# Kernel optimization log

Hardware: AMD Instinct MI355X
Metric: run time of the kernel (lower is better)

Reference implementation:

```python
import jax, jax.numpy as jnp
import numpy as np

N_Q = 16384; N_S = 16384; NN = 32; F_IN = 128; F_OUT = 256
K = 15; DIM = 3
RADIUS = 10.0
KP_EXTENT_CFG = 1.0      # config.NETWORK.KP_EXTENT (also scales learned offsets)
DENSITY = 5.0            # config.NETWORK.DENSITY_PARAMETER
EXTENT = KP_EXTENT_CFG * RADIUS / DENSITY   # 2.0
K_RADIUS = 1.5 * EXTENT
OFFSET_DIM = DIM * (K - 1)  # modulated=False, version=0 -> 42


def setup_inputs() -> dict:
    key = jax.random.key(0)
    ks = jax.random.split(key, 8)
    query_points = jax.random.uniform(ks[0], (N_Q, DIM), dtype=jnp.float32)
    support_points = jax.random.uniform(ks[1], (N_S, DIM), dtype=jnp.float32)
    neighbors = jax.random.randint(ks[2], (N_Q, NN), 0, N_S)
    features = jax.random.normal(ks[3], (N_S, F_IN), dtype=jnp.float32)
    # kernel points: fixed disposition inside ball of radius 1.5*extent, first point at center
    kp = jax.random.normal(ks[4], (K, DIM), dtype=jnp.float32)
    kp = kp / jnp.linalg.norm(kp, axis=1, keepdims=True) * (0.7 * K_RADIUS)
    K_points = kp.at[0].set(0.0)
    weight = jax.random.normal(ks[5], (K, F_IN, F_OUT), dtype=jnp.float32) / np.sqrt(F_IN)
    deformable_weight = jax.random.normal(ks[6], (K, F_IN, OFFSET_DIM), dtype=jnp.float32) / np.sqrt(F_IN)
    bias = jnp.zeros((OFFSET_DIM,), dtype=jnp.float32)
    return {"query_points": query_points, "support_points": support_points,
            "neighbors": neighbors, "features": features, "K_points": K_points,
            "weight": weight, "deformable_weight": deformable_weight, "bias": bias}


def _gather_neighb(query_points, support_points, neighbors, features):
    # pad with shadow point (far away) and zero feature row, as in KPConv_ops
    sp = jnp.concatenate([support_points, jnp.full((1, DIM), 1e6, support_points.dtype)], 0)
    ft = jnp.concatenate([features, jnp.zeros((1, features.shape[1]), features.dtype)], 0)
    rel = sp[neighbors] - query_points[:, None, :]   # [n, nn, 3]
    nfeat = ft[neighbors]                            # [n, nn, f]
    return rel, nfeat


def _linear_influence(sq_dist):
    # KP_INFLUENCE='linear': relu(1 - d/extent); CONVOLUTION_MODE='sum'
    return jnp.maximum(1.0 - jnp.sqrt(sq_dist) / EXTENT, 0.0)


def reference(query_points, support_points, neighbors, features, K_points,
              weight, deformable_weight, bias):
    rel, nfeat = _gather_neighb(query_points, support_points, neighbors, features)

    # --- rigid KPConv producing offsets (version=0) ---
    d0 = rel[:, :, None, :] - K_points[None, None, :, :]   # [n, nn, K, 3]
    sq0 = jnp.sum(d0 * d0, axis=-1)                        # [n, nn, K]
    w0 = _linear_influence(sq0)
    wf0 = jnp.einsum('enk,enf->ekf', w0, nfeat)            # [n, K, f]
    feat0 = jnp.einsum('ekf,kfo->eo', wf0, deformable_weight) + bias  # [n, 42]

    # not modulated: reshape to offsets, prepend zero offset for center kernel point
    offsets = feat0.reshape(-1, K - 1, DIM)
    offsets = jnp.concatenate([jnp.zeros_like(offsets[:, :1, :]), offsets], axis=1)
    offsets = offsets * KP_EXTENT_CFG                      # [n, K, 3]

    # --- deformable KPConv ---
    def_kp = K_points[None, :, :] + offsets                # [n, K, 3]
    d1 = rel[:, :, None, :] - def_kp[:, None, :, :]        # [n, nn, K, 3]
    sq1 = jnp.sum(d1 * d1, axis=-1)                        # [n, nn, K]
    w1 = _linear_influence(sq1)                            # out-of-range neighbors get 0 weight
    wf1 = jnp.einsum('enk,enf->ekf', w1, nfeat)            # [n, K, f]
    out = jnp.einsum('ekf,kfo->eo', wf1, weight)           # [n, f_out]
    return out
```

## Files before the change

kernel.cpp:

```cpp
#include <hip/hip_runtime.h>
#include <hip/hip_bf16.h>
#include <math.h>

typedef __attribute__((ext_vector_type(8))) short bf16x8;
typedef __attribute__((ext_vector_type(4))) float f32x4;

#define NQ 16384
#define NN 32
#define FI 128
#define FO 256
#define KPN 15
#define OD 42
#define INV_EXT 0.5f

#define WS_FP1    0u
#define WS_FP2    (8u * 1024u * 1024u)
#define WS_BSW    (12u * 1024u * 1024u)
#define WS_DWBH   (13u * 1024u * 1024u)
#define WS_DWBL   (WS_DWBH + 196608u)

static __device__ __forceinline__ unsigned short f2bf(float x) {
    union { __hip_bfloat16 h; unsigned short u; } cv;
    cv.h = __float2bfloat16(x);
    return cv.u;
}
static __device__ __forceinline__ float bf2f(unsigned short h) {
    union { unsigned int u; float f; } cv;
    cv.u = ((unsigned int)h) << 16;
    return cv.f;
}

union U8 { unsigned short u[8]; bf16x8 v; };

__global__ void pre_all(const float* __restrict__ feat,
                        unsigned int* __restrict__ fp1, unsigned int* __restrict__ fp2,
                        const float* __restrict__ w, unsigned short* __restrict__ Bsw,
                        const float* __restrict__ dw,
                        unsigned short* __restrict__ dhi, unsigned short* __restrict__ dlo)
{
    const int b = blockIdx.x, t = threadIdx.x;
    if (b < 1024) {
        const int g  = b * 256 + t;
        const int lq = g & 3;
        const int fp = (g >> 2) & 3;
        const int s  = g >> 4;
        const float4* f4 = (const float4*)feat;
        const float4 A = f4[s * 32 + fp * 8 + lq];
        const float4 C = f4[s * 32 + fp * 8 + 4 + lq];
        const float av[4] = {A.x, A.y, A.z, A.w};
        const float cv[4] = {C.x, C.y, C.z, C.w};
        uint4 p1a, p1c, p2;
        unsigned int* pa = (unsigned int*)&p1a;
        unsigned int* pc = (unsigned int*)&p1c;
        unsigned int* p2p = (unsigned int*)&p2;
        #pragma unroll
        for (int e = 0; e < 4; e++) {
            const unsigned short ha = f2bf(av[e]), hc = f2bf(cv[e]);
            const unsigned short la = f2bf(av[e] - bf2f(ha));
            const unsigned short lc = f2bf(cv[e] - bf2f(hc));
            pa[e]  = (unsigned int)ha | ((unsigned int)la << 16);
            pc[e]  = (unsigned int)hc | ((unsigned int)lc << 16);
            p2p[e] = (unsigned int)ha | ((unsigned int)hc << 16);
        }
        *(uint4*)&fp1[s * 128 + fp * 32 + lq * 4]      = p1a;
        *(uint4*)&fp1[s * 128 + fp * 32 + 16 + lq * 4] = p1c;
        *(uint4*)&fp2[s * 64 + fp * 16 + lq * 4]       = p2;
    } else if (b < 1024 + 256) {
        const int tid = (b - 1024) * 256 + t;
        const int lane = tid & 63;
        const int kt   = (tid >> 6) & 63;
        const int nt   = tid >> 12;
        const int n    = nt * 16 + (lane & 15);
        const int kbase = kt * 32 + (lane >> 4) * 8;
        unsigned int p[4];
        #pragma unroll
        for (int jj = 0; jj < 4; jj++) {
            unsigned int lo, hi;
            {
                const int kk = kbase + 2 * jj;
                const int f = kk >> 4, k = kk & 15;
                lo = (k < KPN) ? f2bf(w[(k * FI + f) * FO + n]) : 0u;
            }
            {
                const int kk = kbase + 2 * jj + 1;
                const int f = kk >> 4, k = kk & 15;
                hi = (k < KPN) ? f2bf(w[(k * FI + f) * FO + n]) : 0u;
            }
            p[jj] = lo | (hi << 16);
        }
        unsigned int* op = (unsigned int*)&Bsw[tid * 8];
        op[0] = p[0]; op[1] = p[1]; op[2] = p[2]; op[3] = p[3];
    } else {
        const int tid = (b - 1280) * 256 + t;
        const int lane = tid & 63;
        const int kt   = (tid >> 6) & 63;
        const int nt   = tid >> 12;
        const int o    = nt * 16 + (lane & 15);
        const int kbase = kt * 32 + (lane >> 4) * 8;
        #pragma unroll
        for (int j = 0; j < 8; j++) {
            const int kf = kbase + j;
            const int f = kf >> 4, k = kf & 15;
            float v = (k < KPN && o < OD) ? dw[(k * FI + f) * OD + o] : 0.f;
            unsigned short h = f2bf(v);
            dhi[tid * 8 + j] = h;
            dlo[tid * 8 + j] = f2bf(v - bf2f(h));
        }
    }
}

__global__ __launch_bounds__(512, 4)
void k_fused(const float* __restrict__ query, const float* __restrict__ support,
             const int* __restrict__ neighbors, const unsigned int* __restrict__ fp1,
             const unsigned int* __restrict__ fp2, const float* __restrict__ kpoints,
             const unsigned short* __restrict__ dwB_hi,
             const unsigned short* __restrict__ dwB_lo,
             const unsigned short* __restrict__ Bsw,
             const float* __restrict__ bias, float* __restrict__ out)
{
    __shared__ unsigned short wf[16384];
    __shared__ float relx[1024], rely[1024], relz[1024];
    __shared__ float dk_s[32 * 45];
    __shared__ unsigned short nbr_s[1024];
    __shared__ float kp_s[48];

    const int t = threadIdx.x;
    const int qbase = blockIdx.x * 32;
    if (t < 45) kp_s[t] = kpoints[t];
    if (t >= 45 && t < 48) kp_s[t] = 0.f;

    #pragma unroll
    for (int ii = 0; ii < 2; ii++) {
        const int i = ii * 512 + t;
        const int e = i >> 5, n = i & 31;
        const int q = qbase + e;
        const int idx = neighbors[q * NN + n];
        nbr_s[i] = (unsigned short)idx;
        relx[i] = support[idx * 3 + 0] - query[q * 3 + 0];
        rely[i] = support[idx * 3 + 1] - query[q * 3 + 1];
        relz[i] = support[idx * 3 + 2] - query[q * 3 + 2];
    }
    __syncthreads();

    const int wave = t >> 6, lane = t & 63;
    const int quad = lane >> 4, low = lane & 15;
    const int kb = (low < KPN) ? low * 3 : 0;

    U8 ah[4], al[4];
    {
        const float kx = kp_s[kb + 0], ky = kp_s[kb + 1], kz = kp_s[kb + 2];
        #pragma unroll
        for (int ei = 0; ei < 4; ei++) {
            const int ee = wave * 4 + ei;
            #pragma unroll
            for (int j = 0; j < 8; j++) {
                const int ni = ee * 32 + quad * 8 + j;
                const float dx = relx[ni] - kx;
                const float dy = rely[ni] - ky;
                const float dz = relz[ni] - kz;
                const float d = sqrtf(dx * dx + dy * dy + dz * dz);
                float w = 1.0f - d * INV_EXT;
                w = (low < KPN && w > 0.f) ? w : 0.f;
                const unsigned short h = f2bf(w);
                ah[ei].u[j] = h;
                al[ei].u[j] = f2bf(w - bf2f(h));
            }
        }
    }

    f32x4 acc = {0.f, 0.f, 0.f, 0.f};
    const int et = (wave >= 3) ? 1 : 0;
    const int nt = wave - et * 3;

    for (int c2 = 0; c2 < 8; c2++) {
        #pragma unroll 2
        for (int ei = 0; ei < 4; ei++) {
            const int ee = wave * 4 + ei;
            union { unsigned int u[4]; bf16x8 v; } bh, bl;
            #pragma unroll
            for (int jj = 0; jj < 4; jj++) {
                const int r0 = nbr_s[ee * 32 + quad * 8 + 2 * jj];
                const int r1 = nbr_s[ee * 32 + quad * 8 + 2 * jj + 1];
                const unsigned int g0 = fp1[r0 * 128 + c2 * 16 + low];
                const unsigned int g1 = fp1[r1 * 128 + c2 * 16 + low];
                bh.u[jj] = __builtin_amdgcn_perm(g1, g0, 0x05040100u);
                bl.u[jj] = __builtin_amdgcn_perm(g1, g0, 0x07060302u);
            }
            f32x4 o = {0.f, 0.f, 0.f, 0.f};
            o = __builtin_amdgcn_mfma_f32_16x16x32_bf16(al[ei].v, bh.v, o, 0, 0, 0);
            o = __builtin_amdgcn_mfma_f32_16x16x32_bf16(ah[ei].v, bl.v, o, 0, 0, 0);
            o = __builtin_amdgcn_mfma_f32_16x16x32_bf16(ah[ei].v, bh.v, o, 0, 0, 0);
            const int cblk = low + (quad >> 1) * 16;
            const int slot = ee ^ low;
            const int hw   = cblk * 256 + slot * 8 + (quad & 1) * 4;
            const unsigned short h0 = f2bf(o[0]), h1 = f2bf(o[1]);
            const unsigned short h2 = f2bf(o[2]), h3 = f2bf(o[3]);
            uint2 ph;
            ph.x = (unsigned int)h0 | ((unsigned int)h1 << 16);
            ph.y = (unsigned int)h2 | ((unsigned int)h3 << 16);
            *(uint2*)&wf[hw] = ph;
            uint2 pl;
            pl.x = (unsigned int)f2bf(o[0] - bf2f(h0)) |
                   ((unsigned int)f2bf(o[1] - bf2f(h1)) << 16);
            pl.y = (unsigned int)f2bf(o[2] - bf2f(h2)) |
                   ((unsigned int)f2bf(o[3] - bf2f(h3)) << 16);
            *(uint2*)&wf[8192 + hw] = pl;
        }
        __syncthreads();
        if (wave < 6) {
            const bf16x8* Bh = (const bf16x8*)dwB_hi;
            const bf16x8* Bl = (const bf16x8*)dwB_lo;
            #pragma unroll 4
            for (int ktl = 0; ktl < 8; ktl++) {
                const int fl   = ktl * 2 + (quad >> 1);
                const int cblk = fl + (quad & 1) * 16;
                const int slot = (et * 16 + low) ^ fl;
                const int hw   = cblk * 256 + slot * 8;
                bf16x8 a_h = *(const bf16x8*)&wf[hw];
                bf16x8 a_l = *(const bf16x8*)&wf[8192 + hw];
                const int ktg = c2 * 8 + ktl;
                bf16x8 b_h = Bh[(nt * 64 + ktg) * 64 + lane];
                bf16x8 b_l = Bl[(nt * 64 + ktg) * 64 + lane];
                acc = __builtin_amdgcn_mfma_f32_16x16x32_bf16(a_l, b_h, acc, 0, 0, 0);
                acc = __builtin_amdgcn_mfma_f32_16x16x32_bf16(a_h, b_l, acc, 0, 0, 0);
                acc = __builtin_amdgcn_mfma_f32_16x16x32_bf16(a_h, b_h, acc, 0, 0, 0);
            }
        } else if (c2 == 0) {
            const int idx2 = (wave - 6) * 64 + lane;
            if (idx2 < 96) dk_s[(idx2 / 3) * 45 + (idx2 % 3)] = kp_s[idx2 % 3];
        }
        __syncthreads();
    }

    if (wave < 6) {
        const int o = nt * 16 + low;
        if (o < OD) {
            const float bo = bias[o] + kp_s[3 + o];
            #pragma unroll
            for (int r = 0; r < 4; r++) {
                const int ee = et * 16 + quad * 4 + r;
                dk_s[ee * 45 + 3 + o] = bo + acc[r];
            }
        }
    }
    __syncthreads();

    U8 af[4];
    #pragma unroll
    for (int ei = 0; ei < 4; ei++) {
        const int ee = wave * 4 + ei;
        const float kx = dk_s[ee * 45 + kb + 0];
        const float ky = dk_s[ee * 45 + kb + 1];
        const float kz = dk_s[ee * 45 + kb + 2];
        #pragma unroll
        for (int j = 0; j < 8; j++) {
            const int ni = ee * 32 + quad * 8 + j;
            const float dx = relx[ni] - kx;
            const float dy = rely[ni] - ky;
            const float dz = relz[ni] - kz;
            const float d = sqrtf(dx * dx + dy * dy + dz * dz);
            float w = 1.0f - d * INV_EXT;
            w = (low < KPN && w > 0.f) ? w : 0.f;
            af[ei].u[j] = f2bf(w);
        }
    }

    f32x4 acc00 = {0,0,0,0}, acc01 = {0,0,0,0};
    f32x4 acc10 = {0,0,0,0}, acc11 = {0,0,0,0};
    const int nt0 = wave * 2, nt1 = nt0 + 1;
    const bf16x8* Bp = (const bf16x8*)Bsw;

    for (int c = 0; c < 4; c++) {
        #pragma unroll
        for (int ei = 0; ei < 4; ei++) {
            const int ee = wave * 4 + ei;
            union { unsigned int u[4]; bf16x8 v; } bA, bB;
            #pragma unroll
            for (int jj = 0; jj < 4; jj++) {
                const int r0 = nbr_s[ee * 32 + quad * 8 + 2 * jj];
                const int r1 = nbr_s[ee * 32 + quad * 8 + 2 * jj + 1];
                const unsigned int d0 = fp2[r0 * 64 + c * 16 + low];
                const unsigned int d1 = fp2[r1 * 64 + c * 16 + low];
                bA.u[jj] = __builtin_amdgcn_perm(d1, d0, 0x05040100u);
                bB.u[jj] = __builtin_amdgcn_perm(d1, d0, 0x07060302u);
            }
            #pragma unroll
            for (int hh2 = 0; hh2 < 2; hh2++) {
                const bf16x8 b = hh2 ? bB.v : bA.v;
                f32x4 o = {0.f, 0.f, 0.f, 0.f};
                o = __builtin_amdgcn_mfma_f32_16x16x32_bf16(af[ei].v, b, o, 0, 0, 0);
                const int fc   = hh2 * 16 + low;
                const int cblk = fc + (quad >> 1) * 32;
                const int slot = ee ^ fc;
                const int hw   = cblk * 256 + slot * 8 + (quad & 1) * 4;
                uint2 ph;
                ph.x = (unsigned int)f2bf(o[0]) | ((unsigned int)f2bf(o[1]) << 16);
                ph.y = (unsigned int)f2bf(o[2]) | ((unsigned int)f2bf(o[3]) << 16);
                *(uint2*)&wf[hw] = ph;
            }
        }
        __syncthreads();
        #pragma unroll 4
        for (int ktl = 0; ktl < 16; ktl++) {
            const int fcq  = ktl * 2 + (quad >> 1);
            const int cblk = fcq + (quad & 1) * 32;
            const int s0 = (low ^ fcq) * 8;
            const int s1 = ((16 + low) ^ fcq) * 8;
            bf16x8 a0 = *(const bf16x8*)&wf[cblk * 256 + s0];
            bf16x8 a1 = *(const bf16x8*)&wf[cblk * 256 + s1];
            const int ktg = c * 16 + ktl;
            bf16x8 b0 = Bp[(nt0 * 64 + ktg) * 64 + lane];
            bf16x8 b1 = Bp[(nt1 * 64 + ktg) * 64 + lane];
            acc00 = __builtin_amdgcn_mfma_f32_16x16x32_bf16(a0, b0, acc00, 0, 0, 0);
            acc01 = __builtin_amdgcn_mfma_f32_16x16x32_bf16(a0, b1, acc01, 0, 0, 0);
            acc10 = __builtin_amdgcn_mfma_f32_16x16x32_bf16(a1, b0, acc10, 0, 0, 0);
            acc11 = __builtin_amdgcn_mfma_f32_16x16x32_bf16(a1, b1, acc11, 0, 0, 0);
        }
        __syncthreads();
    }

    #pragma unroll
    for (int r = 0; r < 4; r++) {
        const int e0 = quad * 4 + r;
        out[(qbase + e0) * FO + nt0 * 16 + low] = acc00[r];
        out[(qbase + e0) * FO + nt1 * 16 + low] = acc01[r];
        out[(qbase + 16 + e0) * FO + nt0 * 16 + low] = acc10[r];
        out[(qbase + 16 + e0) * FO + nt1 * 16 + low] = acc11[r];
    }
}

extern "C" void kernel_launch(void* const* d_in, const int* in_sizes, int n_in,
                              void* d_out, int out_size, void* d_ws, size_t ws_size,
                              hipStream_t stream) {
    const float* query     = (const float*)d_in[0];
    const float* support   = (const float*)d_in[1];
    const int*   neighbors = (const int*)  d_in[2];
    const float* features  = (const float*)d_in[3];
    const float* kpoints   = (const float*)d_in[4];
    const float* weight    = (const float*)d_in[5];
    const float* dweight   = (const float*)d_in[6];
    const float* bias      = (const float*)d_in[7];
    float*       out       = (float*)d_out;

    char* ws = (char*)d_ws;
    unsigned int*   fp1  = (unsigned int*)(ws + WS_FP1);
    unsigned int*   fp2  = (unsigned int*)(ws + WS_FP2);
    unsigned short* Bsw  = (unsigned short*)(ws + WS_BSW);
    unsigned short* dwBh = (unsigned short*)(ws + WS_DWBH);
    unsigned short* dwBl = (unsigned short*)(ws + WS_DWBL);

    pre_all<<<1328, 256, 0, stream>>>(features, fp1, fp2, weight, Bsw,
                                      dweight, dwBh, dwBl);
    k_fused<<<NQ / 32, 512, 0, stream>>>(query, support, neighbors, fp1, fp2,
                                         kpoints, dwBh, dwBl, Bsw, bias, out);
}
```

Baseline: 203.1 us.

## Widen neighbor feature gathers to 8 bytes and split each chunk in two

The preprocessing kernel now interleaves the packed bf16 feature layouts so that two adjacent feature chunks sit in one 8-byte word. Both gather loops (the hi/lo split pass and the bf16 pass) now issue uint2 loads covering two chunks at once. The second half is held in registers and consumed after an extra barrier, so the number of scattered global gather instructions is halved. The cost is more live registers per thread (32 extra dwords of held gathered data), which may reduce occupancy.

Measured after the change: 205.4 us. No clear change (+1.2%).

```diff
diff --git a/kernel.cpp b/kernel.cpp
--- a/kernel.cpp
+++ b/kernel.cpp
@@ -49,22 +49,19 @@
         const float4 C = f4[s * 32 + fp * 8 + 4 + lq];
         const float av[4] = {A.x, A.y, A.z, A.w};
         const float cv[4] = {C.x, C.y, C.z, C.w};
-        uint4 p1a, p1c, p2;
-        unsigned int* pa = (unsigned int*)&p1a;
-        unsigned int* pc = (unsigned int*)&p1c;
-        unsigned int* p2p = (unsigned int*)&p2;
+        unsigned int pw[8];
         #pragma unroll
         for (int e = 0; e < 4; e++) {
             const unsigned short ha = f2bf(av[e]), hc = f2bf(cv[e]);
             const unsigned short la = f2bf(av[e] - bf2f(ha));
             const unsigned short lc = f2bf(cv[e] - bf2f(hc));
-            pa[e]  = (unsigned int)ha | ((unsigned int)la << 16);
-            pc[e]  = (unsigned int)hc | ((unsigned int)lc << 16);
-            p2p[e] = (unsigned int)ha | ((unsigned int)hc << 16);
-        }
-        *(uint4*)&fp1[s * 128 + fp * 32 + lq * 4]      = p1a;
-        *(uint4*)&fp1[s * 128 + fp * 32 + 16 + lq * 4] = p1c;
-        *(uint4*)&fp2[s * 64 + fp * 16 + lq * 4]       = p2;
+            pw[2 * e]     = (unsigned int)ha | ((unsigned int)hc << 16);
+            pw[2 * e + 1] = (unsigned int)la | ((unsigned int)lc << 16);
+            fp2[s * 64 + (fp >> 1) * 32 + (lq * 4 + e) * 2 + (fp & 1)] =
+                (unsigned int)ha | ((unsigned int)hc << 16);
+        }
+        *(uint4*)&fp1[s * 128 + fp * 32 + lq * 8]     = *(uint4*)&pw[0];
+        *(uint4*)&fp1[s * 128 + fp * 32 + lq * 8 + 4] = *(uint4*)&pw[4];
     } else if (b < 1024 + 256) {
         const int tid = (b - 1024) * 256 + t;
         const int lane = tid & 63;
@@ -172,8 +169,14 @@
     const int et = (wave >= 3) ? 1 : 0;
     const int nt = wave - et * 3;
 
-    for (int c2 = 0; c2 < 8; c2++) {
-        #pragma unroll 2
+    const uint2* fp1v = (const uint2*)fp1;
+    const uint2* fp2v = (const uint2*)fp2;
+    const bf16x8* Bh = (const bf16x8*)dwB_hi;
+    const bf16x8* Bl = (const bf16x8*)dwB_lo;
+
+    for (int c2 = 0; c2 < 4; c2++) {
+        unsigned int rbh[4][4], rbl[4][4];
+        #pragma unroll
         for (int ei = 0; ei < 4; ei++) {
             const int ee = wave * 4 + ei;
             union { unsigned int u[4]; bf16x8 v; } bh, bl;
@@ -181,10 +184,12 @@
             for (int jj = 0; jj < 4; jj++) {
                 const int r0 = nbr_s[ee * 32 + quad * 8 + 2 * jj];
                 const int r1 = nbr_s[ee * 32 + quad * 8 + 2 * jj + 1];
-                const unsigned int g0 = fp1[r0 * 128 + c2 * 16 + low];
-                const unsigned int g1 = fp1[r1 * 128 + c2 * 16 + low];
-                bh.u[jj] = __builtin_amdgcn_perm(g1, g0, 0x05040100u);
-                bl.u[jj] = __builtin_amdgcn_perm(g1, g0, 0x07060302u);
+                const uint2 d0 = fp1v[r0 * 64 + c2 * 16 + low];
+                const uint2 d1 = fp1v[r1 * 64 + c2 * 16 + low];
+                bh.u[jj]    = __builtin_amdgcn_perm(d1.x, d0.x, 0x05040100u);
+                rbh[ei][jj] = __builtin_amdgcn_perm(d1.x, d0.x, 0x07060302u);
+                bl.u[jj]    = __builtin_amdgcn_perm(d1.y, d0.y, 0x05040100u);
+                rbl[ei][jj] = __builtin_amdgcn_perm(d1.y, d0.y, 0x07060302u);
             }
             f32x4 o = {0.f, 0.f, 0.f, 0.f};
             o = __builtin_amdgcn_mfma_f32_16x16x32_bf16(al[ei].v, bh.v, o, 0, 0, 0);
@@ -208,8 +213,6 @@
         }
         __syncthreads();
         if (wave < 6) {
-            const bf16x8* Bh = (const bf16x8*)dwB_hi;
-            const bf16x8* Bl = (const bf16x8*)dwB_lo;
             #pragma unroll 4
             for (int ktl = 0; ktl < 8; ktl++) {
                 const int fl   = ktl * 2 + (quad >> 1);
@@ -218,7 +221,7 @@
                 const int hw   = cblk * 256 + slot * 8;
                 bf16x8 a_h = *(const bf16x8*)&wf[hw];
                 bf16x8 a_l = *(const bf16x8*)&wf[8192 + hw];
-                const int ktg = c2 * 8 + ktl;
+                const int ktg = (2 * c2) * 8 + ktl;
                 bf16x8 b_h = Bh[(nt * 64 + ktg) * 64 + lane];
                 bf16x8 b_l = Bl[(nt * 64 + ktg) * 64 + lane];
                 acc = __builtin_amdgcn_mfma_f32_16x16x32_bf16(a_l, b_h, acc, 0, 0, 0);
@@ -228,6 +231,53 @@
         } else if (c2 == 0) {
             const int idx2 = (wave - 6) * 64 + lane;
             if (idx2 < 96) dk_s[(idx2 / 3) * 45 + (idx2 % 3)] = kp_s[idx2 % 3];
+        }
+        __syncthreads();
+        #pragma unroll
+        for (int ei = 0; ei < 4; ei++) {
+            const int ee = wave * 4 + ei;
+            union { unsigned int u[4]; bf16x8 v; } bh, bl;
+            bh.u[0] = rbh[ei][0]; bh.u[1] = rbh[ei][1];
+            bh.u[2] = rbh[ei][2]; bh.u[3] = rbh[ei][3];
+            bl.u[0] = rbl[ei][0]; bl.u[1] = rbl[ei][1];
+            bl.u[2] = rbl[ei][2]; bl.u[3] = rbl[ei][3];
+            f32x4 o = {0.f, 0.f, 0.f, 0.f};
+            o = __builtin_amdgcn_mfma_f32_16x16x32_bf16(al[ei].v, bh.v, o, 0, 0, 0);
+            o = __builtin_amdgcn_mfma_f32_16x16x32_bf16(ah[ei].v, bl.v, o, 0, 0, 0);
+            o = __builtin_amdgcn_mfma_f32_16x16x32_bf16(ah[ei].v, bh.v, o, 0, 0, 0);
+            const int cblk = low + (quad >> 1) * 16;
+            const int slot = ee ^ low;
+            const int hw   = cblk * 256 + slot * 8 + (quad & 1) * 4;
+            const unsigned short h0 = f2bf(o[0]), h1 = f2bf(o[1]);
+            const unsigned short h2 = f2bf(o[2]), h3 = f2bf(o[3]);
+            uint2 ph;
+            ph.x = (unsigned int)h0 | ((unsigned int)h1 << 16);
+            ph.y = (unsigned int)h2 | ((unsigned int)h3 << 16);
+            *(uint2*)&wf[hw] = ph;
+            uint2 pl;
+            pl.x = (unsigned int)f2bf(o[0] - bf2f(h0)) |
+                   ((unsigned int)f2bf(o[1] - bf2f(h1)) << 16);
+            pl.y = (unsigned int)f2bf(o[2] - bf2f(h2)) |
+                   ((unsigned int)f2bf(o[3] - bf2f(h3)) << 16);
+            *(uint2*)&wf[8192 + hw] = pl;
+        }
+        __syncthreads();
+        if (wave < 6) {
+            #pragma unroll 4
+            for (int ktl = 0; ktl < 8; ktl++) {
+                const int fl   = ktl * 2 + (quad >> 1);
+                const int cblk = fl + (quad & 1) * 16;
+                const int slot = (et * 16 + low) ^ fl;
+                const int hw   = cblk * 256 + slot * 8;
+                bf16x8 a_h = *(const bf16x8*)&wf[hw];
+                bf16x8 a_l = *(const bf16x8*)&wf[8192 + hw];
+                const int ktg = (2 * c2 + 1) * 8 + ktl;
+                bf16x8 b_h = Bh[(nt * 64 + ktg) * 64 + lane];
+                bf16x8 b_l = Bl[(nt * 64 + ktg) * 64 + lane];
+                acc = __builtin_amdgcn_mfma_f32_16x16x32_bf16(a_l, b_h, acc, 0, 0, 0);
+                acc = __builtin_amdgcn_mfma_f32_16x16x32_bf16(a_h, b_l, acc, 0, 0, 0);
+                acc = __builtin_amdgcn_mfma_f32_16x16x32_bf16(a_h, b_h, acc, 0, 0, 0);
+            }
         }
         __syncthreads();
     }
@@ -270,7 +320,8 @@
     const int nt0 = wave * 2, nt1 = nt0 + 1;
     const bf16x8* Bp = (const bf16x8*)Bsw;
 
-    for (int c = 0; c < 4; c++) {
+    for (int c2 = 0; c2 < 2; c2++) {
+        unsigned int rA[4][4], rB[4][4];
         #pragma unroll
         for (int ei = 0; ei < 4; ei++) {
             const int ee = wave * 4 + ei;
@@ -279,10 +330,12 @@
             for (int jj = 0; jj < 4; jj++) {
                 const int r0 = nbr_s[ee * 32 + quad * 8 + 2 * jj];
                 const int r1 = nbr_s[ee * 32 + quad * 8 + 2 * jj + 1];
-                const unsigned int d0 = fp2[r0 * 64 + c * 16 + low];
-                const unsigned int d1 = fp2[r1 * 64 + c * 16 + low];
-                bA.u[jj] = __builtin_amdgcn_perm(d1, d0, 0x05040100u);
-                bB.u[jj] = __builtin_amdgcn_perm(d1, d0, 0x07060302u);
+                const uint2 g0 = fp2v[r0 * 32 + c2 * 16 + low];
+                const uint2 g1 = fp2v[r1 * 32 + c2 * 16 + low];
+                bA.u[jj]   = __builtin_amdgcn_perm(g1.x, g0.x, 0x05040100u);
+                bB.u[jj]   = __builtin_amdgcn_perm(g1.x, g0.x, 0x07060302u);
+                rA[ei][jj] = __builtin_amdgcn_perm(g1.y, g0.y, 0x05040100u);
+                rB[ei][jj] = __builtin_amdgcn_perm(g1.y, g0.y, 0x07060302u);
             }
             #pragma unroll
             for (int hh2 = 0; hh2 < 2; hh2++) {
@@ -308,7 +361,48 @@
             const int s1 = ((16 + low) ^ fcq) * 8;
             bf16x8 a0 = *(const bf16x8*)&wf[cblk * 256 + s0];
             bf16x8 a1 = *(const bf16x8*)&wf[cblk * 256 + s1];
-            const int ktg = c * 16 + ktl;
+            const int ktg = (2 * c2) * 16 + ktl;
+            bf16x8 b0 = Bp[(nt0 * 64 + ktg) * 64 + lane];
+            bf16x8 b1 = Bp[(nt1 * 64 + ktg) * 64 + lane];
+            acc00 = __builtin_amdgcn_mfma_f32_16x16x32_bf16(a0, b0, acc00, 0, 0, 0);
+            acc01 = __builtin_amdgcn_mfma_f32_16x16x32_bf16(a0, b1, acc01, 0, 0, 0);
+            acc10 = __builtin_amdgcn_mfma_f32_16x16x32_bf16(a1, b0, acc10, 0, 0, 0);
+            acc11 = __builtin_amdgcn_mfma_f32_16x16x32_bf16(a1, b1, acc11, 0, 0, 0);
+        }
+        __syncthreads();
+        #pragma unroll
+        for (int ei = 0; ei < 4; ei++) {
+            const int ee = wave * 4 + ei;
+            union { unsigned int u[4]; bf16x8 v; } bA, bB;
+            bA.u[0] = rA[ei][0]; bA.u[1] = rA[ei][1];
+            bA.u[2] = rA[ei][2]; bA.u[3] = rA[ei][3];
+            bB.u[0] = rB[ei][0]; bB.u[1] = rB[ei][1];
+            bB.u[2] = rB[ei][2]; bB.u[3] = rB[ei][3];
+            #pragma unroll
+            for (int hh2 = 0; hh2 < 2; hh2++) {
+                const bf16x8 b = hh2 ? bB.v : bA.v;
+                f32x4 o = {0.f, 0.f, 0.f, 0.f};
+                o = __builtin_amdgcn_mfma_f32_16x16x32_bf16(af[ei].v, b, o, 0, 0, 0);
+                const int fc   = hh2 * 16 + low;
+                const int cblk = fc + (quad >> 1) * 32;
+                const int slot = ee ^ fc;
+                const int hw   = cblk * 256 + slot * 8 + (quad & 1) * 4;
+                uint2 ph;
+                ph.x = (unsigned int)f2bf(o[0]) | ((unsigned int)f2bf(o[1]) << 16);
+                ph.y = (unsigned int)f2bf(o[2]) | ((unsigned int)f2bf(o[3]) << 16);
+                *(uint2*)&wf[hw] = ph;
+            }
+        }
+        __syncthreads();
+        #pragma unroll 4
+        for (int ktl = 0; ktl < 16; ktl++) {
+            const int fcq  = ktl * 2 + (quad >> 1);
+            const int cblk = fcq + (quad & 1) * 32;
+            const int s0 = (low ^ fcq) * 8;
+            const int s1 = ((16 + low) ^ fcq) * 8;
+            bf16x8 a0 = *(const bf16x8*)&wf[cblk * 256 + s0];
+            bf16x8 a1 = *(const bf16x8*)&wf[cblk * 256 + s1];
+            const int ktg = (2 * c2 + 1) * 16 + ktl;
             bf16x8 b0 = Bp[(nt0 * 64 + ktg) * 64 + lane];
             bf16x8 b1 = Bp[(nt1 * 64 + ktg) * 64 + lane];
             acc00 = __builtin_amdgcn_mfma_f32_16x16x32_bf16(a0, b0, acc00, 0, 0, 0);
```
